# Optimization experiments

Hardware: AMD Instinct MI355X
Metric: run time of the kernel (lower is better)

The kernel has to match this reference:

```python
import jax, jax.numpy as jnp
import numpy as np

B, N, CIN, DIM = 4, 16384, 32, 256
NPOINT, NNEIGH = 2048, 16
BN_EPS = 1e-5


def setup_inputs() -> dict:
    key = jax.random.key(0)
    ks = jax.random.split(key, 6)
    return {
        "xyz": jax.random.normal(ks[0], (B, N, 3), jnp.float32),
        "points": jax.random.normal(ks[1], (B, N, CIN), jnp.float32),
        "fc1_w": jax.random.normal(ks[2], (CIN, DIM), jnp.float32) * 0.05,
        "fc1_b": jnp.zeros((DIM,), jnp.float32),
        "conv1_w": jax.random.normal(ks[3], (DIM, DIM), jnp.float32) * 0.05,
        "conv1_b": jnp.zeros((DIM,), jnp.float32),
        "conv2_w": jax.random.normal(ks[4], (DIM, DIM), jnp.float32) * 0.05,
        "conv2_b": jnp.zeros((DIM,), jnp.float32),
        "bn1_g": jnp.ones((DIM,), jnp.float32),
        "bn1_b": jnp.zeros((DIM,), jnp.float32),
        "bn2_g": jnp.ones((DIM,), jnp.float32),
        "bn2_b": jnp.zeros((DIM,), jnp.float32),
        "bn_g": jnp.ones((DIM,), jnp.float32),
        "bn_b": jnp.zeros((DIM,), jnp.float32),
        "npoint": NPOINT,
        "nneigh": NNEIGH,
    }


def _gather(p, i):
    # p: [B, N, ...], i: [B, ...int] -> per-batch fancy index
    return jax.vmap(lambda a, b: a[b])(p, i)


def _batchnorm(x, g, b):
    # x: [B, S, C]; torch BatchNorm1d training-mode forward over (B, S)
    m = x.mean((0, 1), keepdims=True)
    v = x.var((0, 1), keepdims=True)  # biased variance, as torch uses in forward
    return (x - m) * jax.lax.rsqrt(v + BN_EPS) * g + b


def _fps(xyz, npoint):
    # furthest point sampling, seeded at index 0 (pointnet2_utils convention)
    Bn, Nn, _ = xyz.shape
    dist0 = jnp.full((Bn, Nn), jnp.inf, xyz.dtype)
    far0 = jnp.zeros((Bn,), jnp.int32)

    def step(carry, _):
        dist, far = carry
        cent = _gather(xyz, far)  # [B, 3]
        d = jnp.sum((xyz - cent[:, None, :]) ** 2, axis=-1)  # [B, N]
        dist = jnp.minimum(dist, d)
        nxt = jnp.argmax(dist, axis=-1).astype(jnp.int32)
        return (dist, nxt), far

    _, idx = jax.lax.scan(step, (dist0, far0), None, length=npoint)
    return idx.T  # [B, npoint]


def _square_distance(a, b):
    # a: [B, S, 3], b: [B, N, 3] -> [B, S, N]
    return (jnp.sum(a * a, -1)[..., :, None]
            + jnp.sum(b * b, -1)[..., None, :]
            - 2.0 * jnp.einsum('bsc,bnc->bsn', a, b))


def reference(xyz, points, fc1_w, fc1_b, conv1_w, conv1_b, conv2_w, conv2_b,
              bn1_g, bn1_b, bn2_g, bn2_b, bn_g, bn_b, npoint, nneigh):
    fps_idx = _fps(jax.lax.stop_gradient(xyz), npoint)          # [B, S]
    new_xyz = _gather(xyz, fps_idx)                              # [B, S, 3]

    h = points @ fc1_w + fc1_b                                   # [B, N, D]
    points_ori = _gather(h, fps_idx)                             # [B, S, D]

    t = jax.nn.relu(_batchnorm(h @ conv1_w.T + conv1_b, bn1_g, bn1_b))
    h = h + jax.nn.relu(_batchnorm(t @ conv2_w.T + conv2_b, bn2_g, bn2_b))

    d = _square_distance(jax.lax.stop_gradient(new_xyz), jax.lax.stop_gradient(xyz))
    _, idx = jax.lax.top_k(-d, nneigh)                           # [B, S, K] smallest dists
    grouped = _gather(h, idx)                                    # [B, S, K, D]
    new_points = points_ori + grouped.max(axis=2)                # [B, S, D]
    new_points = _batchnorm(new_points, bn_g, bn_b)
    return new_xyz, new_points
```

## Files before the change

### kernel.cpp

```cpp
#include <hip/hip_runtime.h>
#include <math.h>

#define Bn   4
#define Nn   16384
#define CINn 32
#define DIMn 256
#define Sn   2048
#define KNEI 16
#define BNEPS 1e-5f
#define MROWS (Bn * Nn)
#define SROWS (Bn * Sn)

#define NWORK 248
#define NBLK  (NWORK + Bn)

typedef float f32x2 __attribute__((ext_vector_type(2)));

struct FusedSync {
    unsigned stage[8];
    unsigned prog[Bn];
};

#define UMAX_DPP(v, ctl, rmask)                                               \
    {                                                                         \
        unsigned _o = (unsigned)__builtin_amdgcn_update_dpp(                  \
            0, (int)(v), (ctl), (rmask), 0xf, true);                          \
        (v) = ((v) > _o) ? (v) : _o;                                          \
    }
#define WAVE_UMAX64(v)                                                        \
    UMAX_DPP(v, 0x111, 0xf) UMAX_DPP(v, 0x112, 0xf) UMAX_DPP(v, 0x114, 0xf)  \
    UMAX_DPP(v, 0x118, 0xf) UMAX_DPP(v, 0x142, 0xa) UMAX_DPP(v, 0x143, 0xc)
#define U64MAX_DPP16(khi, klo, ctl)                                           \
    {                                                                         \
        unsigned _lo2 = (unsigned)__builtin_amdgcn_update_dpp(                \
            0, (int)(klo), (ctl), 0xf, 0xf, true);                            \
        unsigned _hi2 = (unsigned)__builtin_amdgcn_update_dpp(                \
            0, (int)(khi), (ctl), 0xf, 0xf, true);                            \
        const bool _g = (_hi2 > (khi)) || (_hi2 == (khi) && _lo2 > (klo));    \
        (khi) = _g ? _hi2 : (khi);                                            \
        (klo) = _g ? _lo2 : (klo);                                            \
    }

__global__ __launch_bounds__(64) void fps_zero_kernel(unsigned* __restrict__ s)
{
    if (threadIdx.x < 12) s[threadIdx.x] = 0u;
}

template <bool BT, bool AFF>
__device__ void gemm_team(const float* A, const float* Bm, const float* bias,
                          const float* asc, const float* ash, float* C,
                          int K, int tile, bool act, float* lAs, float* lBs,
                          int ts)
{
    const int tx = ts & 15;
    const int ty = ts >> 4;
    const int r0 = (tile >> 2) * 64;
    const int c0 = (tile & 3) * 64;
    const int rrA = ts >> 2;
    const int kkA = (ts & 3) * 4;
    float acc[4][4] = {};
    for (int kc = 0; kc < K; kc += 16) {
        if (act) {
            const float4 v = *reinterpret_cast<const float4*>(
                &A[(size_t)(r0 + rrA) * K + kc + kkA]);
            const float vv[4] = {v.x, v.y, v.z, v.w};
#pragma unroll
            for (int m = 0; m < 4; ++m) {
                float xv = vv[m];
                if (AFF) {
                    const int k = kc + kkA + m;
                    xv = fmaxf(fmaf(xv, asc[k], ash[k]), 0.0f);
                }
                lAs[(kkA + m) * 64 + rrA] = xv;
            }
            if (BT) {
                const float4 u = *reinterpret_cast<const float4*>(
                    &Bm[(size_t)(c0 + rrA) * K + kc + kkA]);
                lBs[(kkA + 0) * 64 + rrA] = u.x;
                lBs[(kkA + 1) * 64 + rrA] = u.y;
                lBs[(kkA + 2) * 64 + rrA] = u.z;
                lBs[(kkA + 3) * 64 + rrA] = u.w;
            } else {
                const int kk = ts >> 4;
                const int cc = (ts & 15) * 4;
                const float4 u = *reinterpret_cast<const float4*>(
                    &Bm[(size_t)(kc + kk) * DIMn + c0 + cc]);
                *reinterpret_cast<float4*>(&lBs[kk * 64 + cc]) = u;
            }
        }
        __syncthreads();
        if (act) {
#pragma unroll
            for (int kk = 0; kk < 16; ++kk) {
                const float4 a = *reinterpret_cast<const float4*>(&lAs[kk * 64 + ty * 4]);
                const float4 bv = *reinterpret_cast<const float4*>(&lBs[kk * 64 + tx * 4]);
                const float av[4] = {a.x, a.y, a.z, a.w};
                const float bw[4] = {bv.x, bv.y, bv.z, bv.w};
#pragma unroll
                for (int i = 0; i < 4; ++i)
#pragma unroll
                    for (int j = 0; j < 4; ++j)
                        acc[i][j] = fmaf(av[i], bw[j], acc[i][j]);
            }
        }
        __syncthreads();
    }
    if (act) {
        const int c = c0 + tx * 4;
#pragma unroll
        for (int i = 0; i < 4; ++i) {
            float4 o;
            o.x = acc[i][0] + bias[c + 0];
            o.y = acc[i][1] + bias[c + 1];
            o.z = acc[i][2] + bias[c + 2];
            o.w = acc[i][3] + bias[c + 3];
            *reinterpret_cast<float4*>(&C[(size_t)(r0 + ty * 4 + i) * DIMn + c]) = o;
        }
    }
}

__device__ inline void stage_sync(unsigned* ctr, int t)
{
    __syncthreads();
    if (t == 0) {
        __hip_atomic_fetch_add(ctr, 1u, __ATOMIC_RELEASE, __HIP_MEMORY_SCOPE_AGENT);
        while (__hip_atomic_load(ctr, __ATOMIC_ACQUIRE, __HIP_MEMORY_SCOPE_AGENT)
               < (unsigned)NWORK)
            __builtin_amdgcn_s_sleep(2);
    }
    __syncthreads();
}

__global__ __launch_bounds__(1024, 1) void fused_kernel(
    const float* __restrict__ xyz, const float* __restrict__ points,
    const float* __restrict__ fc1_w, const float* __restrict__ fc1_b,
    const float* __restrict__ conv1_w, const float* __restrict__ conv1_b,
    const float* __restrict__ conv2_w, const float* __restrict__ conv2_b,
    const float* __restrict__ bn1_g, const float* __restrict__ bn1_b,
    const float* __restrict__ bn2_g, const float* __restrict__ bn2_b,
    float* __restrict__ h0, float* __restrict__ A1, float* __restrict__ A2,
    float* __restrict__ pre, int* __restrict__ fidx,
    float* __restrict__ ps, float* __restrict__ pq, float* __restrict__ scv,
    float* __restrict__ newxyz, FusedSync* sync)
{
    __shared__ __align__(16) char smem[131072];
    __shared__ unsigned long long s_aux[33];
    __shared__ float s_wz[2][16];
    __shared__ __align__(16) float4 s_obuf[256];
    __shared__ int s_nidx[KNEI];
    const int t = threadIdx.x;

    if (blockIdx.x < Bn) {
#pragma clang fp contract(off)
        float4* s_xy4 = reinterpret_cast<float4*>(smem);
        unsigned long long (*s_wk)[16] =
            reinterpret_cast<unsigned long long (*)[16]>(s_aux);
        const int b = blockIdx.x;
        const int w = t >> 6;
        const int lane = t & 63;
        const float* __restrict__ px = xyz + (size_t)b * Nn * 3;
        f32x2 z2[8], dist2[8];
#pragma unroll
        for (int jp = 0; jp < 8; ++jp) {
            const int u = jp * 1024 + t;
            const float2 q0 = *reinterpret_cast<const float2*>(&px[6 * u + 0]);
            const float2 q1 = *reinterpret_cast<const float2*>(&px[6 * u + 2]);
            const float2 q2 = *reinterpret_cast<const float2*>(&px[6 * u + 4]);
            float4 pk; pk.x = q0.x; pk.y = q1.y; pk.z = q0.y; pk.w = q2.x;
            s_xy4[u] = pk;
            z2[jp] = f32x2{q1.x, q2.y};
            dist2[jp] = f32x2{__builtin_huge_valf(), __builtin_huge_valf()};
        }
#pragma unroll
        for (int p = 0; p < 8; ++p) asm volatile("" : "+v"(z2[p]));
        float cx = px[0], cy = px[1], cz = px[2];
        if (t == 0) {
            float4 o0; o0.x = cx; o0.y = cy; o0.z = cz; o0.w = __int_as_float(0);
            s_obuf[0] = o0;
        }
        __syncthreads();
        for (int i = 0; i < Sn - 1; ++i) {
            const f32x2 cx2 = {cx, cx}, cy2 = {cy, cy}, cz2 = {cz, cz};
            float bd = -1.0f;
#pragma unroll
            for (int jp = 0; jp < 8; ++jp) {
                const float4 q = s_xy4[jp * 1024 + t];
                const f32x2 dx = f32x2{q.x, q.y} - cx2;
                const f32x2 dy = f32x2{q.z, q.w} - cy2;
                const f32x2 dz = z2[jp] - cz2;
                const f32x2 dd = (dx * dx + dy * dy) + dz * dz;
                const float n0 = fminf(dist2[jp].x, dd.x);
                const float n1 = fminf(dist2[jp].y, dd.y);
                dist2[jp] = f32x2{n0, n1};
                bd = fmaxf(bd, fmaxf(n0, n1));
            }
            unsigned bn = 0;
            float zb = 0.0f;
#pragma unroll
            for (int jp = 7; jp >= 0; --jp) {
                const unsigned n0 = 2u * (unsigned)(jp * 1024 + t);
                if (dist2[jp].y == bd) { bn = 0xFFFFFFFFu - (n0 + 1); zb = z2[jp].y; }
                if (dist2[jp].x == bd) { bn = 0xFFFFFFFFu - n0;       zb = z2[jp].x; }
            }
            const unsigned bdu = __float_as_uint(bd);
            unsigned m = bdu;
            WAVE_UMAX64(m)
            const unsigned bdw = (unsigned)__builtin_amdgcn_readlane((int)m, 63);
            unsigned q2 = (bdu == bdw) ? bn : 0u;
            WAVE_UMAX64(q2)
            const unsigned bnw = (unsigned)__builtin_amdgcn_readlane((int)q2, 63);
            const unsigned long long wmask = __ballot(bdu == bdw && bn == bnw);
            const int wl = __ffsll((unsigned long long)wmask) - 1;
            const float zw = __shfl(zb, wl);
            if (lane == 0) {
                s_wk[i & 1][w] = ((unsigned long long)bdw << 32) | bnw;
                s_wz[i & 1][w] = zw;
            }
            __syncthreads();
            const unsigned long long kk = (lane < 16) ? s_wk[i & 1][lane] : 0ull;
            unsigned klo = (unsigned)kk;
            unsigned khi = (unsigned)(kk >> 32);
            U64MAX_DPP16(khi, klo, 0x111)
            U64MAX_DPP16(khi, klo, 0x112)
            U64MAX_DPP16(khi, klo, 0x114)
            U64MAX_DPP16(khi, klo, 0x118)
            const unsigned bnf = (unsigned)__builtin_amdgcn_readlane((int)klo, 15);
            const int wu = (int)(0xFFFFFFFFu - bnf);
            const int up = wu >> 1;
            const int ww = (up & 1023) >> 6;
            const float4 qw = s_xy4[up];
            cx = (wu & 1) ? qw.y : qw.x;
            cy = (wu & 1) ? qw.w : qw.z;
            cz = s_wz[i & 1][ww];
            if (t == 0) {
                float4 ob; ob.x = cx; ob.y = cy; ob.z = cz;
                ob.w = __int_as_float(wu);
                s_obuf[(i + 1) & 255] = ob;
            }
            if (((i + 2) & 255) == 0) {
                __syncthreads();
                const int cb = (i + 1) - 255;
                if (t < 256) {
                    const float4 v = s_obuf[t];
                    const int bs = b * Sn + cb + t;
                    newxyz[(size_t)bs * 3 + 0] = v.x;
                    newxyz[(size_t)bs * 3 + 1] = v.y;
                    newxyz[(size_t)bs * 3 + 2] = v.z;
                    fidx[bs] = __float_as_int(v.w);
                }
                __syncthreads();
                if (t == 0)
                    __hip_atomic_store(&sync->prog[b], (unsigned)(i + 2),
                                       __ATOMIC_RELEASE, __HIP_MEMORY_SCOPE_AGENT);
            }
        }
        return;
    }

    const int wid = blockIdx.x - Bn;
    const int team = t >> 8;
    const int ts = t & 255;
    float* lAs = reinterpret_cast<float*>(smem) + team * 2048;
    float* lBs = lAs + 1024;
    float* sc1 = scv, *sh1 = scv + 256, *sc2 = scv + 512, *sh2 = scv + 768;

    for (int it = 0; it < 5; ++it) {
        const int tile = it * (NWORK * 4) + wid * 4 + team;
        gemm_team<false, false>(points, fc1_w, fc1_b, nullptr, nullptr, h0,
                                CINn, tile, tile < 4096, lAs, lBs, ts);
    }
    stage_sync(&sync->stage[0], t);
    for (int it = 0; it < 5; ++it) {
        const int tile = it * (NWORK * 4) + wid * 4 + team;
        gemm_team<true, false>(h0, conv1_w, conv1_b, nullptr, nullptr, A1,
                               DIMn, tile, tile < 4096, lAs, lBs, ts);
    }
    stage_sync(&sync->stage[1], t);
    for (int sb = wid; sb < 256; sb += NWORK) {
        if (t < DIMn) {
            float s = 0.0f, q = 0.0f;
            const size_t r0 = (size_t)sb * 256;
            for (int r = 0; r < 256; ++r) {
                const float v = A1[(r0 + r) * DIMn + t];
                s += v;
                q = fmaf(v, v, q);
            }
            ps[sb * DIMn + t] = s;
            pq[sb * DIMn + t] = q;
        }
    }
    stage_sync(&sync->stage[2], t);
    if (wid == 0 && t < DIMn) {
        float s = 0.0f, q = 0.0f;
        for (int i = 0; i < 256; ++i) { s += ps[i * DIMn + t]; q += pq[i * DIMn + t]; }
        const float invN = 1.0f / MROWS;
        const float mean = s * invN;
        const float var = q * invN - mean * mean;
        const float r = 1.0f / sqrtf(var + BNEPS);
        const float scale = bn1_g[t] * r;
        sc1[t] = scale;
        sh1[t] = bn1_b[t] - mean * scale;
    }
    stage_sync(&sync->stage[3], t);
    for (int it = 0; it < 5; ++it) {
        const int tile = it * (NWORK * 4) + wid * 4 + team;
        gemm_team<true, true>(A1, conv2_w, conv2_b, sc1, sh1, A2,
                              DIMn, tile, tile < 4096, lAs, lBs, ts);
    }
    stage_sync(&sync->stage[4], t);
    for (int sb = wid; sb < 256; sb += NWORK) {
        if (t < DIMn) {
            float s = 0.0f, q = 0.0f;
            const size_t r0 = (size_t)sb * 256;
            for (int r = 0; r < 256; ++r) {
                const float v = A2[(r0 + r) * DIMn + t];
                s += v;
                q = fmaf(v, v, q);
            }
            ps[sb * DIMn + t] = s;
            pq[sb * DIMn + t] = q;
        }
    }
    stage_sync(&sync->stage[5], t);
    if (wid == 0 && t < DIMn) {
        float s = 0.0f, q = 0.0f;
        for (int i = 0; i < 256; ++i) { s += ps[i * DIMn + t]; q += pq[i * DIMn + t]; }
        const float invN = 1.0f / MROWS;
        const float mean = s * invN;
        const float var = q * invN - mean * mean;
        const float r = 1.0f / sqrtf(var + BNEPS);
        const float scale = bn2_g[t] * r;
        sc2[t] = scale;
        sh2[t] = bn2_b[t] - mean * scale;
    }
    stage_sync(&sync->stage[6], t);
    for (size_t idx = (size_t)wid * 1024 + t; idx < (size_t)MROWS * DIMn / 4;
         idx += (size_t)NWORK * 1024) {
        const int c4 = (int)(idx & 63);
        const float4 hv = reinterpret_cast<const float4*>(h0)[idx];
        float4 av = reinterpret_cast<float4*>(A2)[idx];
        const float4 s4 = reinterpret_cast<const float4*>(sc2)[c4];
        const float4 b4 = reinterpret_cast<const float4*>(sh2)[c4];
        av.x = hv.x + fmaxf(fmaf(av.x, s4.x, b4.x), 0.0f);
        av.y = hv.y + fmaxf(fmaf(av.y, s4.y, b4.y), 0.0f);
        av.z = hv.z + fmaxf(fmaf(av.z, s4.z, b4.z), 0.0f);
        av.w = hv.w + fmaxf(fmaf(av.w, s4.w, b4.w), 0.0f);
        reinterpret_cast<float4*>(A2)[idx] = av;
    }
    stage_sync(&sync->stage[7], t);

    {
#pragma clang fp contract(off)
        unsigned* s_key = reinterpret_cast<unsigned*>(smem);
        const int b = wid & 3;
        const int w = t >> 6;
        const int lane = t & 63;
        const float* px = xyz + (size_t)b * Nn * 3;
        unsigned cprog = 0;
        for (int q = wid; q < SROWS; q += NWORK) {
            const int s = q >> 2;
            if (t == 0 && cprog < (unsigned)(s + 1)) {
                unsigned p;
                do {
                    p = __hip_atomic_load(&sync->prog[b], __ATOMIC_ACQUIRE,
                                          __HIP_MEMORY_SCOPE_AGENT);
                    if (p < (unsigned)(s + 1)) __builtin_amdgcn_s_sleep(8);
                } while (p < (unsigned)(s + 1));
                cprog = p;
            }
            __syncthreads();
            const int bs = b * Sn + s;
            const float qx = newxyz[(size_t)bs * 3 + 0];
            const float qy = newxyz[(size_t)bs * 3 + 1];
            const float qz = newxyz[(size_t)bs * 3 + 2];
            const float qq = (qx * qx + qy * qy) + qz * qz;
            unsigned long long mkey = ~0ull;
#pragma unroll 4
            for (int u = 0; u < 16; ++u) {
                const int n = t + (u << 10);
                const float bx = px[n * 3 + 0];
                const float by = px[n * 3 + 1];
                const float bz = px[n * 3 + 2];
                const float bb2 = (bx * bx + by * by) + bz * bz;
                const float ab = (qx * bx + qy * by) + qz * bz;
                const float d = (qq + bb2) - 2.0f * ab;
                unsigned u32 = __float_as_uint(d);
                u32 = ((int)u32 < 0) ? ~u32 : (u32 | 0x80000000u);
                s_key[n] = u32;
                const unsigned long long k =
                    ((unsigned long long)u32 << 32) | (unsigned)n;
                mkey = (k < mkey) ? k : mkey;
            }
            __syncthreads();
            for (int r = 0; r < KNEI; ++r) {
                unsigned long long k = mkey;
#pragma unroll
                for (int off = 32; off > 0; off >>= 1) {
                    const unsigned long long o = __shfl_xor(k, off);
                    k = (o < k) ? o : k;
                }
                if (lane == 0) s_aux[w] = k;
                __syncthreads();
                if (w == 0) {
                    unsigned long long kk = (lane < 16) ? s_aux[lane] : ~0ull;
#pragma unroll
                    for (int off = 8; off > 0; off >>= 1) {
                        const unsigned long long o = __shfl_xor(kk, off);
                        kk = (o < kk) ? o : kk;
                    }
                    if (lane == 0) {
                        s_aux[32] = kk;
                        s_nidx[r] = (int)(unsigned)(kk & 0xFFFFFFFFull);
                    }
                }
                __syncthreads();
                const unsigned long long wk = s_aux[32];
                if (wk == mkey) {
                    const int wn = (int)(unsigned)(wk & 0xFFFFFFFFull);
                    s_key[wn] = 0xFFFFFFFFu;
                    mkey = ~0ull;
#pragma unroll 4
                    for (int u = 0; u < 16; ++u) {
                        const int n = t + (u << 10);
                        const unsigned long long kk2 =
                            ((unsigned long long)s_key[n] << 32) | (unsigned)n;
                        mkey = (kk2 < mkey) ? kk2 : mkey;
                    }
                }
            }
            __syncthreads();
            if (t < DIMn) {
                const int fid = fidx[bs];
                const float po = h0[((size_t)b * Nn + fid) * DIMn + t];
                float m = -__builtin_huge_valf();
#pragma unroll
                for (int r = 0; r < KNEI; ++r) {
                    const int n = s_nidx[r];
                    m = fmaxf(m, A2[((size_t)b * Nn + n) * DIMn + t]);
                }
                pre[(size_t)bs * DIMn + t] = po + m;
            }
            __syncthreads();
        }
    }
}

__global__ __launch_bounds__(256) void stats_partial(const float* __restrict__ X,
                                                     int rowsPerBlk,
                                                     float* __restrict__ ps,
                                                     float* __restrict__ pq)
{
    const int c = threadIdx.x;
    const size_t r0 = (size_t)blockIdx.x * rowsPerBlk;
    float s = 0.0f, q = 0.0f;
    for (int r = 0; r < rowsPerBlk; ++r) {
        const float v = X[(r0 + r) * DIMn + c];
        s += v;
        q = fmaf(v, v, q);
    }
    ps[blockIdx.x * DIMn + c] = s;
    pq[blockIdx.x * DIMn + c] = q;
}

__global__ __launch_bounds__(256) void bn_finalize(const float* __restrict__ ps,
                                                   const float* __restrict__ pq,
                                                   int nblk, float invN,
                                                   const float* __restrict__ g,
                                                   const float* __restrict__ bb,
                                                   float* __restrict__ sc,
                                                   float* __restrict__ sh)
{
    const int c = threadIdx.x;
    float s = 0.0f, q = 0.0f;
    for (int i = 0; i < nblk; ++i) {
        s += ps[i * DIMn + c];
        q += pq[i * DIMn + c];
    }
    const float mean = s * invN;
    const float var = q * invN - mean * mean;
    const float r = 1.0f / sqrtf(var + BNEPS);
    const float scale = g[c] * r;
    sc[c] = scale;
    sh[c] = bb[c] - mean * scale;
}

__global__ __launch_bounds__(256) void apply_bn_kernel(const float* __restrict__ pre,
                                                       const float* __restrict__ sc,
                                                       const float* __restrict__ sh,
                                                       float* __restrict__ out)
{
    const size_t i = (size_t)blockIdx.x * 256 + threadIdx.x;
    const int c4 = (int)(i & 63);
    const float4 v = reinterpret_cast<const float4*>(pre)[i];
    const float4 s4 = reinterpret_cast<const float4*>(sc)[c4];
    const float4 b4 = reinterpret_cast<const float4*>(sh)[c4];
    float4 o;
    o.x = fmaf(v.x, s4.x, b4.x);
    o.y = fmaf(v.y, s4.y, b4.y);
    o.z = fmaf(v.z, s4.z, b4.z);
    o.w = fmaf(v.w, s4.w, b4.w);
    reinterpret_cast<float4*>(out)[i] = o;
}

extern "C" void kernel_launch(void* const* d_in, const int* in_sizes, int n_in,
                              void* d_out, int out_size, void* d_ws, size_t ws_size,
                              hipStream_t stream)
{
    (void)in_sizes; (void)n_in; (void)out_size; (void)ws_size;
    const float* xyz     = (const float*)d_in[0];
    const float* points  = (const float*)d_in[1];
    const float* fc1_w   = (const float*)d_in[2];
    const float* fc1_b   = (const float*)d_in[3];
    const float* conv1_w = (const float*)d_in[4];
    const float* conv1_b = (const float*)d_in[5];
    const float* conv2_w = (const float*)d_in[6];
    const float* conv2_b = (const float*)d_in[7];
    const float* bn1_g   = (const float*)d_in[8];
    const float* bn1_b   = (const float*)d_in[9];
    const float* bn2_g   = (const float*)d_in[10];
    const float* bn2_b   = (const float*)d_in[11];
    const float* bn_g    = (const float*)d_in[12];
    const float* bn_b    = (const float*)d_in[13];

    float* out = (float*)d_out;
    float* newxyz = out;
    float* outpts = out + (size_t)Bn * Sn * 3;

    char* w = (char*)d_ws;
    float* h0   = (float*)(w);
    float* A1   = (float*)(w + (64ull << 20));
    float* A2   = (float*)(w + (128ull << 20));
    float* pre  = (float*)(w + (192ull << 20));
    int*   fidx = (int*)  (w + (200ull << 20));
    float* ps   = (float*)(w + (201ull << 20));
    float* pq   = ps + 256 * 256;
    float* scv  = pq + 256 * 256;
    float* sc3  = scv + 1024;
    float* sh3  = sc3 + 256;
    FusedSync* sync = (FusedSync*)(w + (203ull << 20));

    fps_zero_kernel<<<1, 64, 0, stream>>>((unsigned*)sync);
    fused_kernel<<<NBLK, 1024, 0, stream>>>(
        xyz, points, fc1_w, fc1_b, conv1_w, conv1_b, conv2_w, conv2_b,
        bn1_g, bn1_b, bn2_g, bn2_b, h0, A1, A2, pre, fidx, ps, pq, scv,
        newxyz, sync);
    stats_partial<<<64, 256, 0, stream>>>(pre, SROWS / 64, ps, pq);
    bn_finalize<<<1, 256, 0, stream>>>(ps, pq, 64, 1.0f / SROWS, bn_g, bn_b, sc3, sh3);
    apply_bn_kernel<<<(SROWS * DIMn / 4) / 256, 256, 0, stream>>>(pre, sc3, sh3, outpts);
}
```

Measured before the change: 3.825 ms.

## Halve FPS block active waves and fold final batchnorm into fused kernel

The furthest-point-sampling blocks now run only 8 active waves, each thread holding 16 points instead of 8. This shrinks the per-iteration cross-wave reduction and its output buffer. The stats, finalize and apply passes of the final batchnorm move into the persistent fused kernel behind extra grid-wide barriers, which removes three separate kernel launches. The trade-off is more serial work per thread in the FPS loop and more spin-barrier stages inside the fused kernel.

```diff
diff --git a/kernel.cpp b/kernel.cpp
--- a/kernel.cpp
+++ b/kernel.cpp
@@ -17,7 +17,7 @@
 typedef float f32x2 __attribute__((ext_vector_type(2)));
 
 struct FusedSync {
-    unsigned stage[8];
+    unsigned stage[12];
     unsigned prog[Bn];
 };
 
@@ -43,7 +43,7 @@
 
 __global__ __launch_bounds__(64) void fps_zero_kernel(unsigned* __restrict__ s)
 {
-    if (threadIdx.x < 12) s[threadIdx.x] = 0u;
+    if (threadIdx.x < 16) s[threadIdx.x] = 0u;
 }
 
 template <bool BT, bool AFF>
@@ -138,109 +138,116 @@
     const float* __restrict__ conv2_w, const float* __restrict__ conv2_b,
     const float* __restrict__ bn1_g, const float* __restrict__ bn1_b,
     const float* __restrict__ bn2_g, const float* __restrict__ bn2_b,
+    const float* __restrict__ bn3_g, const float* __restrict__ bn3_b,
     float* __restrict__ h0, float* __restrict__ A1, float* __restrict__ A2,
     float* __restrict__ pre, int* __restrict__ fidx,
     float* __restrict__ ps, float* __restrict__ pq, float* __restrict__ scv,
-    float* __restrict__ newxyz, FusedSync* sync)
+    float* __restrict__ newxyz, float* __restrict__ outpts, FusedSync* sync)
 {
     __shared__ __align__(16) char smem[131072];
     __shared__ unsigned long long s_aux[33];
-    __shared__ float s_wz[2][16];
-    __shared__ __align__(16) float4 s_obuf[256];
+    __shared__ float s_wz[2][8];
+    __shared__ __align__(16) float4 s_obuf[64];
     __shared__ int s_nidx[KNEI];
     const int t = threadIdx.x;
 
     if (blockIdx.x < Bn) {
 #pragma clang fp contract(off)
         float4* s_xy4 = reinterpret_cast<float4*>(smem);
-        unsigned long long (*s_wk)[16] =
-            reinterpret_cast<unsigned long long (*)[16]>(s_aux);
+        unsigned long long (*s_wk)[8] =
+            reinterpret_cast<unsigned long long (*)[8]>(s_aux);
         const int b = blockIdx.x;
         const int w = t >> 6;
         const int lane = t & 63;
+        const bool act = t < 512;
         const float* __restrict__ px = xyz + (size_t)b * Nn * 3;
-        f32x2 z2[8], dist2[8];
-#pragma unroll
-        for (int jp = 0; jp < 8; ++jp) {
-            const int u = jp * 1024 + t;
-            const float2 q0 = *reinterpret_cast<const float2*>(&px[6 * u + 0]);
-            const float2 q1 = *reinterpret_cast<const float2*>(&px[6 * u + 2]);
-            const float2 q2 = *reinterpret_cast<const float2*>(&px[6 * u + 4]);
-            float4 pk; pk.x = q0.x; pk.y = q1.y; pk.z = q0.y; pk.w = q2.x;
-            s_xy4[u] = pk;
-            z2[jp] = f32x2{q1.x, q2.y};
-            dist2[jp] = f32x2{__builtin_huge_valf(), __builtin_huge_valf()};
-        }
-#pragma unroll
-        for (int p = 0; p < 8; ++p) asm volatile("" : "+v"(z2[p]));
+        f32x2 z2[16], dist2[16];
         float cx = px[0], cy = px[1], cz = px[2];
+        if (act) {
+#pragma unroll
+            for (int jp = 0; jp < 16; ++jp) {
+                const int u = jp * 512 + t;
+                const float2 q0 = *reinterpret_cast<const float2*>(&px[6 * u + 0]);
+                const float2 q1 = *reinterpret_cast<const float2*>(&px[6 * u + 2]);
+                const float2 q2 = *reinterpret_cast<const float2*>(&px[6 * u + 4]);
+                float4 pk; pk.x = q0.x; pk.y = q1.y; pk.z = q0.y; pk.w = q2.x;
+                s_xy4[u] = pk;
+                z2[jp] = f32x2{q1.x, q2.y};
+                dist2[jp] = f32x2{__builtin_huge_valf(), __builtin_huge_valf()};
+            }
+#pragma unroll
+            for (int p = 0; p < 16; ++p) asm volatile("" : "+v"(z2[p]));
+        }
         if (t == 0) {
             float4 o0; o0.x = cx; o0.y = cy; o0.z = cz; o0.w = __int_as_float(0);
             s_obuf[0] = o0;
         }
         __syncthreads();
         for (int i = 0; i < Sn - 1; ++i) {
-            const f32x2 cx2 = {cx, cx}, cy2 = {cy, cy}, cz2 = {cz, cz};
-            float bd = -1.0f;
-#pragma unroll
-            for (int jp = 0; jp < 8; ++jp) {
-                const float4 q = s_xy4[jp * 1024 + t];
-                const f32x2 dx = f32x2{q.x, q.y} - cx2;
-                const f32x2 dy = f32x2{q.z, q.w} - cy2;
-                const f32x2 dz = z2[jp] - cz2;
-                const f32x2 dd = (dx * dx + dy * dy) + dz * dz;
-                const float n0 = fminf(dist2[jp].x, dd.x);
-                const float n1 = fminf(dist2[jp].y, dd.y);
-                dist2[jp] = f32x2{n0, n1};
-                bd = fmaxf(bd, fmaxf(n0, n1));
-            }
-            unsigned bn = 0;
-            float zb = 0.0f;
-#pragma unroll
-            for (int jp = 7; jp >= 0; --jp) {
-                const unsigned n0 = 2u * (unsigned)(jp * 1024 + t);
-                if (dist2[jp].y == bd) { bn = 0xFFFFFFFFu - (n0 + 1); zb = z2[jp].y; }
-                if (dist2[jp].x == bd) { bn = 0xFFFFFFFFu - n0;       zb = z2[jp].x; }
-            }
-            const unsigned bdu = __float_as_uint(bd);
-            unsigned m = bdu;
-            WAVE_UMAX64(m)
-            const unsigned bdw = (unsigned)__builtin_amdgcn_readlane((int)m, 63);
-            unsigned q2 = (bdu == bdw) ? bn : 0u;
-            WAVE_UMAX64(q2)
-            const unsigned bnw = (unsigned)__builtin_amdgcn_readlane((int)q2, 63);
-            const unsigned long long wmask = __ballot(bdu == bdw && bn == bnw);
-            const int wl = __ffsll((unsigned long long)wmask) - 1;
-            const float zw = __shfl(zb, wl);
-            if (lane == 0) {
-                s_wk[i & 1][w] = ((unsigned long long)bdw << 32) | bnw;
-                s_wz[i & 1][w] = zw;
+            if (act) {
+                const f32x2 cx2 = {cx, cx}, cy2 = {cy, cy}, cz2 = {cz, cz};
+                float bd = -1.0f;
+#pragma unroll
+                for (int jp = 0; jp < 16; ++jp) {
+                    const float4 q = s_xy4[jp * 512 + t];
+                    const f32x2 dx = f32x2{q.x, q.y} - cx2;
+                    const f32x2 dy = f32x2{q.z, q.w} - cy2;
+                    const f32x2 dz = z2[jp] - cz2;
+                    const f32x2 dd = (dx * dx + dy * dy) + dz * dz;
+                    const float n0 = fminf(dist2[jp].x, dd.x);
+                    const float n1 = fminf(dist2[jp].y, dd.y);
+                    dist2[jp] = f32x2{n0, n1};
+                    bd = fmaxf(bd, fmaxf(n0, n1));
+                }
+                unsigned bn = 0;
+                float zb = 0.0f;
+#pragma unroll
+                for (int jp = 15; jp >= 0; --jp) {
+                    const unsigned n0 = 2u * (unsigned)(jp * 512 + t);
+                    if (dist2[jp].y == bd) { bn = 0xFFFFFFFFu - (n0 + 1); zb = z2[jp].y; }
+                    if (dist2[jp].x == bd) { bn = 0xFFFFFFFFu - n0;       zb = z2[jp].x; }
+                }
+                const unsigned bdu = __float_as_uint(bd);
+                unsigned m = bdu;
+                WAVE_UMAX64(m)
+                const unsigned bdw = (unsigned)__builtin_amdgcn_readlane((int)m, 63);
+                unsigned q2 = (bdu == bdw) ? bn : 0u;
+                WAVE_UMAX64(q2)
+                const unsigned bnw = (unsigned)__builtin_amdgcn_readlane((int)q2, 63);
+                const unsigned long long wmask = __ballot(bdu == bdw && bn == bnw);
+                const int wl = __ffsll((unsigned long long)wmask) - 1;
+                const float zw = __shfl(zb, wl);
+                if (lane == 0) {
+                    s_wk[i & 1][w] = ((unsigned long long)bdw << 32) | bnw;
+                    s_wz[i & 1][w] = zw;
+                }
             }
             __syncthreads();
-            const unsigned long long kk = (lane < 16) ? s_wk[i & 1][lane] : 0ull;
-            unsigned klo = (unsigned)kk;
-            unsigned khi = (unsigned)(kk >> 32);
-            U64MAX_DPP16(khi, klo, 0x111)
-            U64MAX_DPP16(khi, klo, 0x112)
-            U64MAX_DPP16(khi, klo, 0x114)
-            U64MAX_DPP16(khi, klo, 0x118)
-            const unsigned bnf = (unsigned)__builtin_amdgcn_readlane((int)klo, 15);
-            const int wu = (int)(0xFFFFFFFFu - bnf);
-            const int up = wu >> 1;
-            const int ww = (up & 1023) >> 6;
-            const float4 qw = s_xy4[up];
-            cx = (wu & 1) ? qw.y : qw.x;
-            cy = (wu & 1) ? qw.w : qw.z;
-            cz = s_wz[i & 1][ww];
-            if (t == 0) {
-                float4 ob; ob.x = cx; ob.y = cy; ob.z = cz;
-                ob.w = __int_as_float(wu);
-                s_obuf[(i + 1) & 255] = ob;
-            }
-            if (((i + 2) & 255) == 0) {
+            if (act) {
+                const unsigned long long kk = (lane < 8) ? s_wk[i & 1][lane] : 0ull;
+                unsigned klo = (unsigned)kk;
+                unsigned khi = (unsigned)(kk >> 32);
+                U64MAX_DPP16(khi, klo, 0x111)
+                U64MAX_DPP16(khi, klo, 0x112)
+                U64MAX_DPP16(khi, klo, 0x114)
+                const unsigned bnf = (unsigned)__builtin_amdgcn_readlane((int)klo, 7);
+                const int wu = (int)(0xFFFFFFFFu - bnf);
+                const int up = wu >> 1;
+                const int ww = (up & 511) >> 6;
+                const float4 qw = s_xy4[up];
+                cx = (wu & 1) ? qw.y : qw.x;
+                cy = (wu & 1) ? qw.w : qw.z;
+                cz = s_wz[i & 1][ww];
+                if (t == 0) {
+                    float4 ob; ob.x = cx; ob.y = cy; ob.z = cz;
+                    ob.w = __int_as_float(wu);
+                    s_obuf[(i + 1) & 63] = ob;
+                }
+            }
+            if (((i + 2) & 63) == 0) {
                 __syncthreads();
-                const int cb = (i + 1) - 255;
-                if (t < 256) {
+                const int cb = (i + 1) - 63;
+                if (t < 64) {
                     const float4 v = s_obuf[t];
                     const int bs = b * Sn + cb + t;
                     newxyz[(size_t)bs * 3 + 0] = v.x;
@@ -263,6 +270,7 @@
     float* lAs = reinterpret_cast<float*>(smem) + team * 2048;
     float* lBs = lAs + 1024;
     float* sc1 = scv, *sh1 = scv + 256, *sc2 = scv + 512, *sh2 = scv + 768;
+    float* sc3 = scv + 1024, *sh3 = scv + 1280;
 
     for (int it = 0; it < 5; ++it) {
         const int tile = it * (NWORK * 4) + wid * 4 + team;
@@ -443,63 +451,45 @@
             __syncthreads();
         }
     }
-}
-
-__global__ __launch_bounds__(256) void stats_partial(const float* __restrict__ X,
-                                                     int rowsPerBlk,
-                                                     float* __restrict__ ps,
-                                                     float* __restrict__ pq)
-{
-    const int c = threadIdx.x;
-    const size_t r0 = (size_t)blockIdx.x * rowsPerBlk;
-    float s = 0.0f, q = 0.0f;
-    for (int r = 0; r < rowsPerBlk; ++r) {
-        const float v = X[(r0 + r) * DIMn + c];
-        s += v;
-        q = fmaf(v, v, q);
-    }
-    ps[blockIdx.x * DIMn + c] = s;
-    pq[blockIdx.x * DIMn + c] = q;
-}
-
-__global__ __launch_bounds__(256) void bn_finalize(const float* __restrict__ ps,
-                                                   const float* __restrict__ pq,
-                                                   int nblk, float invN,
-                                                   const float* __restrict__ g,
-                                                   const float* __restrict__ bb,
-                                                   float* __restrict__ sc,
-                                                   float* __restrict__ sh)
-{
-    const int c = threadIdx.x;
-    float s = 0.0f, q = 0.0f;
-    for (int i = 0; i < nblk; ++i) {
-        s += ps[i * DIMn + c];
-        q += pq[i * DIMn + c];
-    }
-    const float mean = s * invN;
-    const float var = q * invN - mean * mean;
-    const float r = 1.0f / sqrtf(var + BNEPS);
-    const float scale = g[c] * r;
-    sc[c] = scale;
-    sh[c] = bb[c] - mean * scale;
-}
-
-__global__ __launch_bounds__(256) void apply_bn_kernel(const float* __restrict__ pre,
-                                                       const float* __restrict__ sc,
-                                                       const float* __restrict__ sh,
-                                                       float* __restrict__ out)
-{
-    const size_t i = (size_t)blockIdx.x * 256 + threadIdx.x;
-    const int c4 = (int)(i & 63);
-    const float4 v = reinterpret_cast<const float4*>(pre)[i];
-    const float4 s4 = reinterpret_cast<const float4*>(sc)[c4];
-    const float4 b4 = reinterpret_cast<const float4*>(sh)[c4];
-    float4 o;
-    o.x = fmaf(v.x, s4.x, b4.x);
-    o.y = fmaf(v.y, s4.y, b4.y);
-    o.z = fmaf(v.z, s4.z, b4.z);
-    o.w = fmaf(v.w, s4.w, b4.w);
-    reinterpret_cast<float4*>(out)[i] = o;
+    stage_sync(&sync->stage[8], t);
+
+    if (wid < 64 && t < DIMn) {
+        float s = 0.0f, q = 0.0f;
+        const size_t r0 = (size_t)wid * 128;
+        for (int r = 0; r < 128; ++r) {
+            const float v = pre[(r0 + r) * DIMn + t];
+            s += v;
+            q = fmaf(v, v, q);
+        }
+        ps[wid * DIMn + t] = s;
+        pq[wid * DIMn + t] = q;
+    }
+    stage_sync(&sync->stage[9], t);
+    if (wid == 0 && t < DIMn) {
+        float s = 0.0f, q = 0.0f;
+        for (int i = 0; i < 64; ++i) { s += ps[i * DIMn + t]; q += pq[i * DIMn + t]; }
+        const float invN = 1.0f / SROWS;
+        const float mean = s * invN;
+        const float var = q * invN - mean * mean;
+        const float r = 1.0f / sqrtf(var + BNEPS);
+        const float scale = bn3_g[t] * r;
+        sc3[t] = scale;
+        sh3[t] = bn3_b[t] - mean * scale;
+    }
+    stage_sync(&sync->stage[10], t);
+    for (size_t idx = (size_t)wid * 1024 + t; idx < (size_t)SROWS * DIMn / 4;
+         idx += (size_t)NWORK * 1024) {
+        const int c4 = (int)(idx & 63);
+        const float4 v = reinterpret_cast<const float4*>(pre)[idx];
+        const float4 s4 = reinterpret_cast<const float4*>(sc3)[c4];
+        const float4 b4 = reinterpret_cast<const float4*>(sh3)[c4];
+        float4 o;
+        o.x = fmaf(v.x, s4.x, b4.x);
+        o.y = fmaf(v.y, s4.y, b4.y);
+        o.z = fmaf(v.z, s4.z, b4.z);
+        o.w = fmaf(v.w, s4.w, b4.w);
+        reinterpret_cast<float4*>(outpts)[idx] = o;
+    }
 }
 
 extern "C" void kernel_launch(void* const* d_in, const int* in_sizes, int n_in,
@@ -535,16 +525,11 @@
     float* ps   = (float*)(w + (201ull << 20));
     float* pq   = ps + 256 * 256;
     float* scv  = pq + 256 * 256;
-    float* sc3  = scv + 1024;
-    float* sh3  = sc3 + 256;
     FusedSync* sync = (FusedSync*)(w + (203ull << 20));
 
     fps_zero_kernel<<<1, 64, 0, stream>>>((unsigned*)sync);
     fused_kernel<<<NBLK, 1024, 0, stream>>>(
         xyz, points, fc1_w, fc1_b, conv1_w, conv1_b, conv2_w, conv2_b,
-        bn1_g, bn1_b, bn2_g, bn2_b, h0, A1, A2, pre, fidx, ps, pq, scv,
-        newxyz, sync);
-    stats_partial<<<64, 256, 0, stream>>>(pre, SROWS / 64, ps, pq);
-    bn_finalize<<<1, 256, 0, stream>>>(ps, pq, 64, 1.0f / SROWS, bn_g, bn_b, sc3, sh3);
-    apply_bn_kernel<<<(SROWS * DIMn / 4) / 256, 256, 0, stream>>>(pre, sc3, sh3, outpts);
+        bn1_g, bn1_b, bn2_g, bn2_b, bn_g, bn_b, h0, A1, A2, pre, fidx,
+        ps, pq, scv, newxyz, outpts, sync);
 }
```

Measured after the change: 3.825 ms. No clear change (-0.0%).
